# Optimization experiments

Hardware: AMD Instinct MI355X
Metric: run time of the kernel (lower is better)

The kernel has to match this reference:

```python
import jax, jax.numpy as jnp
import numpy as np

NUM_CLASSES = 80
CLS_W, BOX_W, OBJ_W = 0.5, 7.5, 1.0
CENTER_RADIUS = 2.5
LABEL_SMOOTH = 0.0
WARMUP = min(1.0, (0 + 1) / 3)  # current_epoch=0, warmup_epochs=3
EPS = 1e-7


def _make_points(img=640, strides=(8, 16, 32)):
    pts, strs = [], []
    for s in strides:
        n = img // s
        ys, xs = np.meshgrid(np.arange(n), np.arange(n), indexing='ij')
        p = np.stack([(xs + 0.5) * s, (ys + 0.5) * s], -1).reshape(-1, 2)
        pts.append(p)
        strs.append(np.full(p.shape[0], s))
    return (np.concatenate(pts).astype(np.float32),
            np.concatenate(strs).astype(np.float32))


def _rand_boxes(key, shape, img=640.0):
    k1, k2 = jax.random.split(key)
    c = jax.random.uniform(k1, shape + (2,), minval=50.0, maxval=img - 50.0)
    half = jax.random.uniform(k2, shape + (2,), minval=8.0, maxval=120.0)
    return jnp.concatenate([c - half, c + half], axis=-1)


def setup_inputs() -> dict:
    key = jax.random.key(0)
    ks = jax.random.split(key, 6)
    B, P, G, C = 16, 8400, 64, NUM_CLASSES
    points_np, strides_np = _make_points()
    return {
        'pred_cls': jax.random.normal(ks[0], (B, P, C), jnp.float32),
        'pred_box': jax.random.normal(ks[1], (B, P, 4), jnp.float32),
        'pred_obj': jax.random.normal(ks[2], (B, P, 1), jnp.float32),
        'decoded_boxes': _rand_boxes(ks[3], (B, P)),
        'points': jnp.asarray(points_np),
        'strides': jnp.asarray(strides_np),
        'gt_boxes': _rand_boxes(ks[4], (B, G)),
        'gt_labels': jax.random.randint(ks[5], (B, G), 0, C, jnp.int32),
    }


def _ciou_loss(b1, b2):
    # b1, b2: [..., 4] in x1y1x2y2. Returns 1 - CIoU per box.
    x1, y1, x2, y2 = b1[..., 0], b1[..., 1], b1[..., 2], b1[..., 3]
    gx1, gy1, gx2, gy2 = b2[..., 0], b2[..., 1], b2[..., 2], b2[..., 3]
    w1, h1 = x2 - x1, y2 - y1
    w2, h2 = gx2 - gx1, gy2 - gy1
    inter = (jnp.clip(jnp.minimum(x2, gx2) - jnp.maximum(x1, gx1), 0.0) *
             jnp.clip(jnp.minimum(y2, gy2) - jnp.maximum(y1, gy1), 0.0))
    union = w1 * h1 + w2 * h2 - inter + EPS
    iou = inter / union
    cw = jnp.maximum(x2, gx2) - jnp.minimum(x1, gx1)
    ch = jnp.maximum(y2, gy2) - jnp.minimum(y1, gy1)
    c2 = cw * cw + ch * ch + EPS
    rho2 = ((x1 + x2 - gx1 - gx2) ** 2 + (y1 + y2 - gy1 - gy2) ** 2) * 0.25
    v = (4.0 / (jnp.pi ** 2)) * (jnp.arctan(w2 / (h2 + EPS)) -
                                 jnp.arctan(w1 / (h1 + EPS))) ** 2
    alpha = v / (1.0 - iou + v + EPS)
    return 1.0 - (iou - rho2 / c2 - alpha * v)


def _assign(points, strides, gt_boxes):
    # points [P,2], strides [P], gt_boxes [B,G,4] -> fg [B,P], idx [B,P]
    px = points[None, :, None, 0]                 # [1,P,1]
    py = points[None, :, None, 1]
    gx1 = gt_boxes[:, None, :, 0]                 # [B,1,G]
    gy1 = gt_boxes[:, None, :, 1]
    gx2 = gt_boxes[:, None, :, 2]
    gy2 = gt_boxes[:, None, :, 3]
    deltas = jnp.stack([px - gx1, py - gy1, gx2 - px, gy2 - py], -1)  # [B,P,G,4]
    inside_box = jnp.min(deltas, -1) > 0
    cx, cy = (gx1 + gx2) * 0.5, (gy1 + gy2) * 0.5
    radii = strides[None, :, None] * CENTER_RADIUS
    cdeltas = jnp.stack([px - (cx - radii), py - (cy - radii),
                         cx + radii - px, cy + radii - py], -1)
    inside_center = jnp.min(cdeltas, -1) > 0
    fits = jnp.max(deltas, -1) <= strides[None, :, None] * 8.0
    match = inside_box & inside_center & fits
    fallback = inside_box & inside_center
    match = jnp.where(jnp.any(match, -1, keepdims=True), match, fallback)
    areas = ((gt_boxes[..., 2] - gt_boxes[..., 0]) *
             (gt_boxes[..., 3] - gt_boxes[..., 1]))[:, None, :]  # [B,1,G]
    cand = jnp.where(match, areas, jnp.inf)
    matched_idx = jnp.argmin(cand, -1)                            # [B,P]
    fg = jnp.isfinite(jnp.min(cand, -1))
    return fg, matched_idx


def _bce_mean(logits, targets):
    return jnp.mean(jnp.maximum(logits, 0.0) - logits * targets +
                    jnp.log1p(jnp.exp(-jnp.abs(logits))))


def reference(pred_cls, pred_box, pred_obj, decoded_boxes, points, strides,
              gt_boxes, gt_labels):
    dtype = pred_cls.dtype
    fg, midx = _assign(points, strides, gt_boxes)                 # [B,P]
    matched_boxes = jnp.take_along_axis(
        gt_boxes, midx[:, :, None].repeat(4, axis=2), axis=1)      # [B,P,4]
    matched_labels = jnp.take_along_axis(gt_labels, midx, axis=1)  # [B,P]

    # cls target: one-hot (with optional smoothing) at fg points, zeros elsewhere
    one_hot = jax.nn.one_hot(matched_labels, NUM_CLASSES, dtype=dtype)
    if LABEL_SMOOTH > 0.0:
        one_hot = one_hot * (1.0 - LABEL_SMOOTH) + LABEL_SMOOTH / NUM_CLASSES
    cls_target = jnp.where(fg[..., None], one_hot, 0.0)

    # sanitize predicted boxes
    pb = jnp.nan_to_num(decoded_boxes, nan=0.0, posinf=1000.0, neginf=0.0)
    pb = jnp.clip(pb, -1000.0, 1000.0)
    px1, py1 = pb[..., 0], pb[..., 1]
    px2 = jnp.maximum(px1 + 0.001, pb[..., 2])
    py2 = jnp.maximum(py1 + 0.001, pb[..., 3])
    pb = jnp.stack([px1, py1, px2, py2], -1)

    ciou = _ciou_loss(pb, matched_boxes)                          # [B,P]
    ciou = jnp.clip(jnp.nan_to_num(ciou, nan=1.0, posinf=1.0, neginf=1.0), 0.0, 2.0)

    num_fg = jnp.sum(fg.astype(dtype))
    normalizer = jnp.maximum(num_fg, 1.0)
    loss_box = jnp.sum(jnp.where(fg, ciou, 0.0)) / normalizer
    loss_box = jnp.minimum(jnp.nan_to_num(loss_box), 10.0)

    obj_target = jax.lax.stop_gradient(
        jnp.where(fg, jnp.clip(1.0 - ciou, 0.0, 1.0), 0.0))

    loss_cls = jnp.minimum(jnp.nan_to_num(_bce_mean(pred_cls, cls_target)), 10.0)
    loss_obj = jnp.minimum(jnp.nan_to_num(
        _bce_mean(pred_obj[..., 0], obj_target)), 10.0)

    loss_total = CLS_W * loss_cls + (BOX_W * WARMUP) * loss_box + OBJ_W * loss_obj
    loss_total = jnp.minimum(jnp.nan_to_num(loss_total), 10.0)
    return jnp.stack([loss_total, loss_cls, loss_box, loss_obj])
```

## Files before the change

kernel.cpp:

```cpp
#include <hip/hip_runtime.h>
#include <cmath>

#define NCLS 80
#define NB 16
#define NP 8400
#define NG 64
#define CHUNKS 33
#define PBLK (NB * CHUNKS)
#define CBLK 2625
#define N4 (NB * NP * NCLS / 4)
#define EPSF 1e-7f

__device__ __forceinline__ float softplus_bce(float l) {
    float t = __expf(-fabsf(l));
    return fmaxf(l, 0.f) + __logf(1.f + t);
}

__device__ __forceinline__ float sp4(float4 c) {
    return (softplus_bce(c.x) + softplus_bce(c.y)) +
           (softplus_bce(c.z) + softplus_bce(c.w));
}

__device__ __forceinline__ float sanitize_box(float x) {
    if (isnan(x)) return 0.f;
    if (isinf(x)) x = (x > 0.f) ? 1000.f : 0.f;
    return fminf(fmaxf(x, -1000.f), 1000.f);
}

__global__ __launch_bounds__(256) void k1_main(
    const float* __restrict__ pred_cls, const float* __restrict__ pred_obj,
    const float4* __restrict__ decoded, const float2* __restrict__ points,
    const float* __restrict__ strides, const float4* __restrict__ gt_boxes,
    const int* __restrict__ gt_labels,
    double* __restrict__ clsPart, double* __restrict__ pPart)
{
    const int bid = blockIdx.x, tid = threadIdx.x;

    if (bid >= PBLK) {
        const int cb = bid - PBLK;
        const float4* cls4 = (const float4*)pred_cls;
        const int base = cb * 1024 + tid;
        float4 c0 = cls4[base];
        float4 c1 = cls4[base + 256];
        float4 c2 = cls4[base + 512];
        float4 c3 = cls4[base + 768];
        double acc = (double)sp4(c0) + (double)sp4(c1) +
                     (double)sp4(c2) + (double)sp4(c3);

        __shared__ double shc[4];
        for (int off = 32; off; off >>= 1) acc += __shfl_down(acc, off, 64);
        if ((tid & 63) == 0) shc[tid >> 6] = acc;
        __syncthreads();
        if (tid == 0) clsPart[cb] = shc[0] + shc[1] + shc[2] + shc[3];
        return;
    }

    __shared__ float4 gbox[NG];
    __shared__ float garea[NG];
    __shared__ int glab[NG];

    const int b = bid / CHUNKS;
    const int chunk = bid % CHUNKS;
    const int p = chunk * 256 + tid;

    if (tid < NG) {
        float4 gb = gt_boxes[b * NG + tid];
        gbox[tid] = gb;
        garea[tid] = (gb.z - gb.x) * (gb.w - gb.y);
        glab[tid] = gt_labels[b * NG + tid];
    }
    __syncthreads();

    double v1 = 0.0, v2 = 0.0, v3 = 0.0, v4 = 0.0;

    if (p < NP) {
        float2 pt = points[p];
        const float px = pt.x, py = pt.y;
        const float s = strides[p];
        const float r = s * 2.5f;
        const float fit_thr = s * 8.0f;

        unsigned long long match = 0ull, fallback = 0ull;
        #pragma unroll 4
        for (int g = 0; g < NG; ++g) {
            float4 gb = gbox[g];
            float d0 = px - gb.x, d1 = py - gb.y, d2 = gb.z - px, d3 = gb.w - py;
            float dmin = fminf(fminf(d0, d1), fminf(d2, d3));
            float dmax = fmaxf(fmaxf(d0, d1), fmaxf(d2, d3));
            bool ib = dmin > 0.f;
            float cx = (gb.x + gb.z) * 0.5f, cy = (gb.y + gb.w) * 0.5f;
            float c0 = px - (cx - r), c1 = py - (cy - r);
            float c2 = cx + r - px, c3 = cy + r - py;
            float cmin = fminf(fminf(c0, c1), fminf(c2, c3));
            bool fb = ib && (cmin > 0.f);
            bool m = fb && (dmax <= fit_thr);
            unsigned long long bit = 1ull << g;
            if (m) match |= bit;
            if (fb) fallback |= bit;
        }
        unsigned long long mask = match ? match : fallback;

        float lo = pred_obj[b * NP + p];
        float tobj = 0.f;

        if (mask) {
            int best = 0; float bestA = INFINITY;
            unsigned long long mm = mask;
            while (mm) {
                int g = __ffsll((long long)mm) - 1;
                mm &= mm - 1;
                float a = garea[g];
                if (a < bestA) { bestA = a; best = g; }
            }
            v1 = 1.0;

            float4 db = decoded[(size_t)b * NP + p];
            float x1 = sanitize_box(db.x);
            float y1 = sanitize_box(db.y);
            float x2 = fmaxf(x1 + 0.001f, sanitize_box(db.z));
            float y2 = fmaxf(y1 + 0.001f, sanitize_box(db.w));

            float4 g4 = gbox[best];
            float gx1 = g4.x, gy1 = g4.y, gx2 = g4.z, gy2 = g4.w;

            float w1 = x2 - x1, h1 = y2 - y1;
            float w2 = gx2 - gx1, h2 = gy2 - gy1;
            float iw = fmaxf(fminf(x2, gx2) - fmaxf(x1, gx1), 0.f);
            float ih = fmaxf(fminf(y2, gy2) - fmaxf(y1, gy1), 0.f);
            float inter = iw * ih;
            float uni = w1 * h1 + w2 * h2 - inter + EPSF;
            float iou = inter / uni;
            float cw = fmaxf(x2, gx2) - fminf(x1, gx1);
            float ch = fmaxf(y2, gy2) - fminf(y1, gy1);
            float c2d = cw * cw + ch * ch + EPSF;
            float dx = x1 + x2 - gx1 - gx2, dy = y1 + y2 - gy1 - gy2;
            float rho2 = (dx * dx + dy * dy) * 0.25f;
            float da = atanf(w2 / (h2 + EPSF)) - atanf(w1 / (h1 + EPSF));
            float vv = 0.40528473456935108577551785283891f * da * da;
            float alpha = vv / (1.f - iou + vv + EPSF);
            float ciou = 1.f - (iou - rho2 / c2d - alpha * vv);
            if (isnan(ciou) || isinf(ciou)) ciou = 1.f;
            ciou = fminf(fmaxf(ciou, 0.f), 2.f);
            v2 = (double)ciou;
            tobj = fminf(fmaxf(1.f - ciou, 0.f), 1.f);

            v4 = (double)pred_cls[((size_t)b * NP + p) * NCLS + glab[best]];
        }
        v3 = (double)(softplus_bce(lo) - lo * tobj);
    }

    __shared__ double sh[4][4];
    double vals[4] = {v1, v2, v3, v4};
    for (int k = 0; k < 4; ++k) {
        double v = vals[k];
        for (int off = 32; off; off >>= 1) v += __shfl_down(v, off, 64);
        if ((tid & 63) == 0) sh[k][tid >> 6] = v;
    }
    __syncthreads();
    if (tid == 0) {
        #pragma unroll
        for (int k = 0; k < 4; ++k)
            pPart[(size_t)k * PBLK + bid] = sh[k][0] + sh[k][1] + sh[k][2] + sh[k][3];
    }
}

__global__ __launch_bounds__(256) void k2_finalize(
    const double* __restrict__ clsPart, const double* __restrict__ pPart,
    float* __restrict__ out)
{
    const int tid = threadIdx.x;
    double a[5] = {0, 0, 0, 0, 0};
    for (int i = tid; i < CBLK; i += 256) a[0] += clsPart[i];
    #pragma unroll
    for (int k = 0; k < 4; ++k)
        for (int i = tid; i < PBLK; i += 256) a[1 + k] += pPart[(size_t)k * PBLK + i];

    __shared__ double sh2[4];
    __shared__ double tot[5];
    for (int k = 0; k < 5; ++k) {
        double v = a[k];
        for (int off = 32; off; off >>= 1) v += __shfl_down(v, off, 64);
        __syncthreads();
        if ((tid & 63) == 0) sh2[tid >> 6] = v;
        __syncthreads();
        if (tid == 0) tot[k] = sh2[0] + sh2[1] + sh2[2] + sh2[3];
    }
    __syncthreads();
    if (tid == 0) {
        double cls_sum = tot[0], fg_sum = tot[1], box_sum = tot[2],
               obj_sum = tot[3], corr_sum = tot[4];

        float loss_cls = (float)((cls_sum - corr_sum) /
                                 (double)((size_t)NB * NP * NCLS));
        if (isnan(loss_cls)) loss_cls = 0.f;
        loss_cls = fminf(loss_cls, 10.f);

        float numfg = (float)fg_sum;
        float norm = fmaxf(numfg, 1.f);
        float loss_box = (float)box_sum / norm;
        if (isnan(loss_box)) loss_box = 0.f;
        loss_box = fminf(loss_box, 10.f);

        float loss_obj = (float)(obj_sum / (double)(NB * NP));
        if (isnan(loss_obj)) loss_obj = 0.f;
        loss_obj = fminf(loss_obj, 10.f);

        float total = 0.5f * loss_cls + 2.5f * loss_box + loss_obj;
        if (isnan(total)) total = 0.f;
        total = fminf(total, 10.f);

        out[0] = total; out[1] = loss_cls; out[2] = loss_box; out[3] = loss_obj;
    }
}

extern "C" void kernel_launch(void* const* d_in, const int* in_sizes, int n_in,
                              void* d_out, int out_size, void* d_ws, size_t ws_size,
                              hipStream_t stream) {
    const float*  pred_cls  = (const float*)d_in[0];
    const float*  pred_obj  = (const float*)d_in[2];
    const float4* decoded   = (const float4*)d_in[3];
    const float2* points    = (const float2*)d_in[4];
    const float*  strides   = (const float*)d_in[5];
    const float4* gt_boxes  = (const float4*)d_in[6];
    const int*    gt_labels = (const int*)d_in[7];

    double* clsPart = (double*)d_ws;
    double* pPart   = clsPart + CBLK;

    k1_main<<<PBLK + CBLK, 256, 0, stream>>>(
        pred_cls, pred_obj, decoded, points, strides, gt_boxes, gt_labels,
        clsPart, pPart);
    k2_finalize<<<1, 256, 0, stream>>>(clsPart, pPart, (float*)d_out);
}
```

Baseline: 28.65 us.

## Fuse finalize into main kernel via last-block atomic counter, enlarge class chunks

Merges the finalize kernel into the main kernel: every block stores its partial sums with relaxed atomics, bumps a global counter, and the last block to arrive reduces all partials and writes the outputs. The BCE-sum blocks now handle 2560 float4s each instead of 1024, cutting their count from 2625 to 1050. These blocks also move to the front of the grid so the bandwidth-heavy work is scheduled first. This removes one kernel launch and the gap between kernels, but adds a memset launch and relies on relaxed atomics plus a manual waitcnt for cross-block visibility.

```diff
diff --git a/kernel.cpp b/kernel.cpp
--- a/kernel.cpp
+++ b/kernel.cpp
@@ -7,7 +7,8 @@
 #define NG 64
 #define CHUNKS 33
 #define PBLK (NB * CHUNKS)
-#define CBLK 2625
+#define CB 1050
+#define NBLK (CB + PBLK)
 #define N4 (NB * NP * NCLS / 4)
 #define EPSF 1e-7f
 
@@ -27,153 +28,174 @@
     return fminf(fmaxf(x, -1000.f), 1000.f);
 }
 
-__global__ __launch_bounds__(256) void k1_main(
+__device__ __forceinline__ void cstore(double* p, double v) {
+    __hip_atomic_store(p, v, __ATOMIC_RELAXED, __HIP_MEMORY_SCOPE_AGENT);
+}
+__device__ __forceinline__ double cload(const double* p) {
+    return __hip_atomic_load(p, __ATOMIC_RELAXED, __HIP_MEMORY_SCOPE_AGENT);
+}
+
+__global__ __launch_bounds__(256) void kFused(
     const float* __restrict__ pred_cls, const float* __restrict__ pred_obj,
     const float4* __restrict__ decoded, const float2* __restrict__ points,
     const float* __restrict__ strides, const float4* __restrict__ gt_boxes,
     const int* __restrict__ gt_labels,
-    double* __restrict__ clsPart, double* __restrict__ pPart)
+    double* __restrict__ clsPart, double* __restrict__ pPart,
+    unsigned* __restrict__ counter, float* __restrict__ out)
 {
     const int bid = blockIdx.x, tid = threadIdx.x;
 
-    if (bid >= PBLK) {
-        const int cb = bid - PBLK;
+    if (bid < CB) {
         const float4* cls4 = (const float4*)pred_cls;
-        const int base = cb * 1024 + tid;
-        float4 c0 = cls4[base];
-        float4 c1 = cls4[base + 256];
-        float4 c2 = cls4[base + 512];
-        float4 c3 = cls4[base + 768];
-        double acc = (double)sp4(c0) + (double)sp4(c1) +
-                     (double)sp4(c2) + (double)sp4(c3);
+        const int base = bid * 2560 + tid;
+        float4 a0 = cls4[base];
+        float4 a1 = cls4[base + 256];
+        float4 a2 = cls4[base + 512];
+        float4 a3 = cls4[base + 768];
+        float4 a4 = cls4[base + 1024];
+        double acc = (double)sp4(a0) + (double)sp4(a1) + (double)sp4(a2) +
+                     (double)sp4(a3) + (double)sp4(a4);
+        float4 b0 = cls4[base + 1280];
+        float4 b1 = cls4[base + 1536];
+        float4 b2 = cls4[base + 1792];
+        float4 b3 = cls4[base + 2048];
+        float4 b4 = cls4[base + 2304];
+        acc += (double)sp4(b0) + (double)sp4(b1) + (double)sp4(b2) +
+               (double)sp4(b3) + (double)sp4(b4);
 
         __shared__ double shc[4];
         for (int off = 32; off; off >>= 1) acc += __shfl_down(acc, off, 64);
         if ((tid & 63) == 0) shc[tid >> 6] = acc;
         __syncthreads();
-        if (tid == 0) clsPart[cb] = shc[0] + shc[1] + shc[2] + shc[3];
-        return;
-    }
-
-    __shared__ float4 gbox[NG];
-    __shared__ float garea[NG];
-    __shared__ int glab[NG];
-
-    const int b = bid / CHUNKS;
-    const int chunk = bid % CHUNKS;
-    const int p = chunk * 256 + tid;
-
-    if (tid < NG) {
-        float4 gb = gt_boxes[b * NG + tid];
-        gbox[tid] = gb;
-        garea[tid] = (gb.z - gb.x) * (gb.w - gb.y);
-        glab[tid] = gt_labels[b * NG + tid];
+        if (tid == 0) cstore(&clsPart[bid], shc[0] + shc[1] + shc[2] + shc[3]);
+    } else {
+        __shared__ float4 gbox[NG];
+        __shared__ float garea[NG];
+        __shared__ int glab[NG];
+
+        const int pb = bid - CB;
+        const int b = pb / CHUNKS;
+        const int chunk = pb % CHUNKS;
+        const int p = chunk * 256 + tid;
+
+        if (tid < NG) {
+            float4 gb = gt_boxes[b * NG + tid];
+            gbox[tid] = gb;
+            garea[tid] = (gb.z - gb.x) * (gb.w - gb.y);
+            glab[tid] = gt_labels[b * NG + tid];
+        }
+        __syncthreads();
+
+        double v1 = 0.0, v2 = 0.0, v3 = 0.0, v4 = 0.0;
+
+        if (p < NP) {
+            float2 pt = points[p];
+            const float px = pt.x, py = pt.y;
+            const float s = strides[p];
+            const float r = s * 2.5f;
+            const float fit_thr = s * 8.0f;
+
+            unsigned long long match = 0ull, fallback = 0ull;
+            #pragma unroll 4
+            for (int g = 0; g < NG; ++g) {
+                float4 gb = gbox[g];
+                float d0 = px - gb.x, d1 = py - gb.y, d2 = gb.z - px, d3 = gb.w - py;
+                float dmin = fminf(fminf(d0, d1), fminf(d2, d3));
+                float dmax = fmaxf(fmaxf(d0, d1), fmaxf(d2, d3));
+                bool ib = dmin > 0.f;
+                float cx = (gb.x + gb.z) * 0.5f, cy = (gb.y + gb.w) * 0.5f;
+                float c0 = px - (cx - r), c1 = py - (cy - r);
+                float c2 = cx + r - px, c3 = cy + r - py;
+                float cmin = fminf(fminf(c0, c1), fminf(c2, c3));
+                bool fb = ib && (cmin > 0.f);
+                bool m = fb && (dmax <= fit_thr);
+                unsigned long long bit = 1ull << g;
+                if (m) match |= bit;
+                if (fb) fallback |= bit;
+            }
+            unsigned long long mask = match ? match : fallback;
+
+            float lo = pred_obj[b * NP + p];
+            float tobj = 0.f;
+
+            if (mask) {
+                int best = 0; float bestA = INFINITY;
+                unsigned long long mm = mask;
+                while (mm) {
+                    int g = __ffsll((long long)mm) - 1;
+                    mm &= mm - 1;
+                    float a = garea[g];
+                    if (a < bestA) { bestA = a; best = g; }
+                }
+                v1 = 1.0;
+
+                float4 db = decoded[(size_t)b * NP + p];
+                float x1 = sanitize_box(db.x);
+                float y1 = sanitize_box(db.y);
+                float x2 = fmaxf(x1 + 0.001f, sanitize_box(db.z));
+                float y2 = fmaxf(y1 + 0.001f, sanitize_box(db.w));
+
+                float4 g4 = gbox[best];
+                float gx1 = g4.x, gy1 = g4.y, gx2 = g4.z, gy2 = g4.w;
+
+                float w1 = x2 - x1, h1 = y2 - y1;
+                float w2 = gx2 - gx1, h2 = gy2 - gy1;
+                float iw = fmaxf(fminf(x2, gx2) - fmaxf(x1, gx1), 0.f);
+                float ih = fmaxf(fminf(y2, gy2) - fmaxf(y1, gy1), 0.f);
+                float inter = iw * ih;
+                float uni = w1 * h1 + w2 * h2 - inter + EPSF;
+                float iou = inter / uni;
+                float cw = fmaxf(x2, gx2) - fminf(x1, gx1);
+                float ch = fmaxf(y2, gy2) - fminf(y1, gy1);
+                float c2d = cw * cw + ch * ch + EPSF;
+                float dx = x1 + x2 - gx1 - gx2, dy = y1 + y2 - gy1 - gy2;
+                float rho2 = (dx * dx + dy * dy) * 0.25f;
+                float da = atanf(w2 / (h2 + EPSF)) - atanf(w1 / (h1 + EPSF));
+                float vv = 0.40528473456935108577551785283891f * da * da;
+                float alpha = vv / (1.f - iou + vv + EPSF);
+                float ciou = 1.f - (iou - rho2 / c2d - alpha * vv);
+                if (isnan(ciou) || isinf(ciou)) ciou = 1.f;
+                ciou = fminf(fmaxf(ciou, 0.f), 2.f);
+                v2 = (double)ciou;
+                tobj = fminf(fmaxf(1.f - ciou, 0.f), 1.f);
+
+                v4 = (double)pred_cls[((size_t)b * NP + p) * NCLS + glab[best]];
+            }
+            v3 = (double)(softplus_bce(lo) - lo * tobj);
+        }
+
+        __shared__ double sh[4][4];
+        double vals[4] = {v1, v2, v3, v4};
+        for (int k = 0; k < 4; ++k) {
+            double v = vals[k];
+            for (int off = 32; off; off >>= 1) v += __shfl_down(v, off, 64);
+            if ((tid & 63) == 0) sh[k][tid >> 6] = v;
+        }
+        __syncthreads();
+        if (tid == 0) {
+            #pragma unroll
+            for (int k = 0; k < 4; ++k)
+                cstore(&pPart[(size_t)k * PBLK + pb],
+                       sh[k][0] + sh[k][1] + sh[k][2] + sh[k][3]);
+        }
+    }
+
+    __shared__ int lastFlag;
+    if (tid == 0) {
+        asm volatile("s_waitcnt vmcnt(0)" ::: "memory");
+        unsigned old = __hip_atomic_fetch_add(counter, 1u, __ATOMIC_RELAXED,
+                                              __HIP_MEMORY_SCOPE_AGENT);
+        lastFlag = (old == (unsigned)(NBLK - 1)) ? 1 : 0;
     }
     __syncthreads();
-
-    double v1 = 0.0, v2 = 0.0, v3 = 0.0, v4 = 0.0;
-
-    if (p < NP) {
-        float2 pt = points[p];
-        const float px = pt.x, py = pt.y;
-        const float s = strides[p];
-        const float r = s * 2.5f;
-        const float fit_thr = s * 8.0f;
-
-        unsigned long long match = 0ull, fallback = 0ull;
-        #pragma unroll 4
-        for (int g = 0; g < NG; ++g) {
-            float4 gb = gbox[g];
-            float d0 = px - gb.x, d1 = py - gb.y, d2 = gb.z - px, d3 = gb.w - py;
-            float dmin = fminf(fminf(d0, d1), fminf(d2, d3));
-            float dmax = fmaxf(fmaxf(d0, d1), fmaxf(d2, d3));
-            bool ib = dmin > 0.f;
-            float cx = (gb.x + gb.z) * 0.5f, cy = (gb.y + gb.w) * 0.5f;
-            float c0 = px - (cx - r), c1 = py - (cy - r);
-            float c2 = cx + r - px, c3 = cy + r - py;
-            float cmin = fminf(fminf(c0, c1), fminf(c2, c3));
-            bool fb = ib && (cmin > 0.f);
-            bool m = fb && (dmax <= fit_thr);
-            unsigned long long bit = 1ull << g;
-            if (m) match |= bit;
-            if (fb) fallback |= bit;
-        }
-        unsigned long long mask = match ? match : fallback;
-
-        float lo = pred_obj[b * NP + p];
-        float tobj = 0.f;
-
-        if (mask) {
-            int best = 0; float bestA = INFINITY;
-            unsigned long long mm = mask;
-            while (mm) {
-                int g = __ffsll((long long)mm) - 1;
-                mm &= mm - 1;
-                float a = garea[g];
-                if (a < bestA) { bestA = a; best = g; }
-            }
-            v1 = 1.0;
-
-            float4 db = decoded[(size_t)b * NP + p];
-            float x1 = sanitize_box(db.x);
-            float y1 = sanitize_box(db.y);
-            float x2 = fmaxf(x1 + 0.001f, sanitize_box(db.z));
-            float y2 = fmaxf(y1 + 0.001f, sanitize_box(db.w));
-
-            float4 g4 = gbox[best];
-            float gx1 = g4.x, gy1 = g4.y, gx2 = g4.z, gy2 = g4.w;
-
-            float w1 = x2 - x1, h1 = y2 - y1;
-            float w2 = gx2 - gx1, h2 = gy2 - gy1;
-            float iw = fmaxf(fminf(x2, gx2) - fmaxf(x1, gx1), 0.f);
-            float ih = fmaxf(fminf(y2, gy2) - fmaxf(y1, gy1), 0.f);
-            float inter = iw * ih;
-            float uni = w1 * h1 + w2 * h2 - inter + EPSF;
-            float iou = inter / uni;
-            float cw = fmaxf(x2, gx2) - fminf(x1, gx1);
-            float ch = fmaxf(y2, gy2) - fminf(y1, gy1);
-            float c2d = cw * cw + ch * ch + EPSF;
-            float dx = x1 + x2 - gx1 - gx2, dy = y1 + y2 - gy1 - gy2;
-            float rho2 = (dx * dx + dy * dy) * 0.25f;
-            float da = atanf(w2 / (h2 + EPSF)) - atanf(w1 / (h1 + EPSF));
-            float vv = 0.40528473456935108577551785283891f * da * da;
-            float alpha = vv / (1.f - iou + vv + EPSF);
-            float ciou = 1.f - (iou - rho2 / c2d - alpha * vv);
-            if (isnan(ciou) || isinf(ciou)) ciou = 1.f;
-            ciou = fminf(fmaxf(ciou, 0.f), 2.f);
-            v2 = (double)ciou;
-            tobj = fminf(fmaxf(1.f - ciou, 0.f), 1.f);
-
-            v4 = (double)pred_cls[((size_t)b * NP + p) * NCLS + glab[best]];
-        }
-        v3 = (double)(softplus_bce(lo) - lo * tobj);
-    }
-
-    __shared__ double sh[4][4];
-    double vals[4] = {v1, v2, v3, v4};
-    for (int k = 0; k < 4; ++k) {
-        double v = vals[k];
-        for (int off = 32; off; off >>= 1) v += __shfl_down(v, off, 64);
-        if ((tid & 63) == 0) sh[k][tid >> 6] = v;
-    }
-    __syncthreads();
-    if (tid == 0) {
-        #pragma unroll
-        for (int k = 0; k < 4; ++k)
-            pPart[(size_t)k * PBLK + bid] = sh[k][0] + sh[k][1] + sh[k][2] + sh[k][3];
-    }
-}
-
-__global__ __launch_bounds__(256) void k2_finalize(
-    const double* __restrict__ clsPart, const double* __restrict__ pPart,
-    float* __restrict__ out)
-{
-    const int tid = threadIdx.x;
+    if (!lastFlag) return;
+
     double a[5] = {0, 0, 0, 0, 0};
-    for (int i = tid; i < CBLK; i += 256) a[0] += clsPart[i];
+    for (int i = tid; i < CB; i += 256) a[0] += cload(&clsPart[i]);
     #pragma unroll
     for (int k = 0; k < 4; ++k)
-        for (int i = tid; i < PBLK; i += 256) a[1 + k] += pPart[(size_t)k * PBLK + i];
+        for (int i = tid; i < PBLK; i += 256)
+            a[1 + k] += cload(&pPart[(size_t)k * PBLK + i]);
 
     __shared__ double sh2[4];
     __shared__ double tot[5];
@@ -224,11 +246,13 @@
     const float4* gt_boxes  = (const float4*)d_in[6];
     const int*    gt_labels = (const int*)d_in[7];
 
-    double* clsPart = (double*)d_ws;
-    double* pPart   = clsPart + CBLK;
-
-    k1_main<<<PBLK + CBLK, 256, 0, stream>>>(
+    double*   clsPart = (double*)d_ws;
+    double*   pPart   = clsPart + CB;
+    unsigned* counter = (unsigned*)(pPart + 4 * PBLK);
+
+    hipMemsetAsync(counter, 0, sizeof(unsigned), stream);
+
+    kFused<<<NBLK, 256, 0, stream>>>(
         pred_cls, pred_obj, decoded, points, strides, gt_boxes, gt_labels,
-        clsPart, pPart);
-    k2_finalize<<<1, 256, 0, stream>>>(clsPart, pPart, (float*)d_out);
-}
+        clsPart, pPart, counter, (float*)d_out);
+}
```

New measurement: 40.79 us. 42.4% more time.
